# Kernel optimization log

Hardware: AMD Instinct MI355X
Metric: run time of the kernel (lower is better)

The kernel has to match this reference:

```python
import jax, jax.numpy as jnp
import numpy as np

B, T, D, H, F = 4, 2048, 512, 8, 2048
WINDOW = 128
HD = D // H
EPS = 1e-5


def layer_norm(x, g, b):
    mu = jnp.mean(x, axis=-1, keepdims=True)
    var = jnp.mean(jnp.square(x - mu), axis=-1, keepdims=True)
    return (x - mu) * jax.lax.rsqrt(var + EPS) * g + b


def setup_inputs() -> dict:
    key = jax.random.key(0)
    ks = jax.random.split(key, 5)
    s = 0.02
    return {
        "x": jax.random.normal(ks[0], (B, T, D), dtype=jnp.float32),
        "in_proj_w": jax.random.normal(ks[1], (3 * D, D), dtype=jnp.float32) * s,
        "in_proj_b": jnp.zeros((3 * D,), dtype=jnp.float32),
        "out_w": jax.random.normal(ks[2], (D, D), dtype=jnp.float32) * s,
        "out_b": jnp.zeros((D,), dtype=jnp.float32),
        "ln1_g": jnp.ones((D,), dtype=jnp.float32),
        "ln1_b": jnp.zeros((D,), dtype=jnp.float32),
        "ln2_g": jnp.ones((D,), dtype=jnp.float32),
        "ln2_b": jnp.zeros((D,), dtype=jnp.float32),
        "w1": jax.random.normal(ks[3], (F, D), dtype=jnp.float32) * s,
        "b1": jnp.zeros((F,), dtype=jnp.float32),
        "w2": jax.random.normal(ks[4], (D, F), dtype=jnp.float32) * s,
        "b2": jnp.zeros((D,), dtype=jnp.float32),
    }


def reference(x, in_proj_w, in_proj_b, out_w, out_b, ln1_g, ln1_b, ln2_g, ln2_b, w1, b1, w2, b2):
    # pre-norm sliding-window causal self-attention
    x2 = layer_norm(x, ln1_g, ln1_b)
    qkv = x2 @ in_proj_w.T + in_proj_b  # (B,T,3D)
    q, k, v = jnp.split(qkv, 3, axis=-1)
    q = q.reshape(B, T, H, HD)
    k = k.reshape(B, T, H, HD)
    v = v.reshape(B, T, H, HD)
    scale = 1.0 / np.sqrt(HD).astype(np.float32)
    scores = jnp.einsum("bthd,bshd->bhts", q, k) * scale  # dense (B,H,T,T)
    idx = jnp.arange(T)
    i = idx[:, None]
    j = idx[None, :]
    allowed = (j <= i) & (j >= i - WINDOW + 1)  # (T,T) bool, True = attend
    scores = jnp.where(allowed[None, None], scores, -jnp.inf)
    attn = jax.nn.softmax(scores, axis=-1)
    ctx = jnp.einsum("bhts,bshd->bthd", attn, v).reshape(B, T, D)
    attn_out = ctx @ out_w.T + out_b
    x = x + attn_out  # dropout is identity in eval
    # FFN block
    x3 = layer_norm(x, ln2_g, ln2_b)
    h = jax.nn.gelu(x3 @ w1.T + b1, approximate=False)
    x = x + h @ w2.T + b2
    return x
```

## Files before the change

### kernel.cpp

```cpp
#include <hip/hip_runtime.h>
#include <math.h>

constexpr int Bn = 4;
constexpr int Tn = 2048;
constexpr int Dn = 512;
constexpr int Hn = 8;
constexpr int HDn = 64;
constexpr int Fn = 2048;
constexpr int WIN = 128;
constexpr float EPS = 1e-5f;
constexpr int Mrows = Bn * Tn;
constexpr int QKVD = 3 * Dn;

using short8 = __attribute__((ext_vector_type(8))) short;
using f32x4  = __attribute__((ext_vector_type(4))) float;

__device__ __forceinline__ short f2bf(float f) {
    unsigned u = __float_as_uint(f);
    unsigned r = (u + 0x7FFFu + ((u >> 16) & 1u)) >> 16;
    return (short)r;
}

__device__ __forceinline__ float gelu_fast(float v) {
    float u = 1.5957691216f * v * (1.0f + 0.044715f * v * v);
    float t = 1.0f - 2.0f / (__expf(u) + 1.0f);
    return 0.5f * v * (1.0f + t);
}

__device__ __forceinline__ void async16(const short* g, short* l) {
    __builtin_amdgcn_global_load_lds(
        (const __attribute__((address_space(1))) void*)g,
        (__attribute__((address_space(3))) void*)l,
        16, 0, 0);
}

__device__ __forceinline__ void ln_row(const float* __restrict__ xrow,
                                       const float* __restrict__ g,
                                       const float* __restrict__ b,
                                       short* __restrict__ yrow, int lane)
{
    const float4* xr = (const float4*)xrow;
    float4 v0 = xr[lane];
    float4 v1 = xr[lane + 64];
    float s = v0.x + v0.y + v0.z + v0.w + v1.x + v1.y + v1.z + v1.w;
#pragma unroll
    for (int off = 32; off >= 1; off >>= 1) s += __shfl_xor(s, off, 64);
    float mu = s * (1.0f / Dn);
    float d0x = v0.x - mu, d0y = v0.y - mu, d0z = v0.z - mu, d0w = v0.w - mu;
    float d1x = v1.x - mu, d1y = v1.y - mu, d1z = v1.z - mu, d1w = v1.w - mu;
    float q = d0x*d0x + d0y*d0y + d0z*d0z + d0w*d0w
            + d1x*d1x + d1y*d1y + d1z*d1z + d1w*d1w;
#pragma unroll
    for (int off = 32; off >= 1; off >>= 1) q += __shfl_xor(q, off, 64);
    float inv = rsqrtf(q * (1.0f / Dn) + EPS);
    const float4* gr = (const float4*)g;
    const float4* br = (const float4*)b;
    float4 g0 = gr[lane], g1 = gr[lane + 64];
    float4 b0 = br[lane], b1 = br[lane + 64];
    short4 a0, a1;
    a0.x = f2bf(d0x * inv * g0.x + b0.x);
    a0.y = f2bf(d0y * inv * g0.y + b0.y);
    a0.z = f2bf(d0z * inv * g0.z + b0.z);
    a0.w = f2bf(d0w * inv * g0.w + b0.w);
    a1.x = f2bf(d1x * inv * g1.x + b1.x);
    a1.y = f2bf(d1y * inv * g1.y + b1.y);
    a1.z = f2bf(d1z * inv * g1.z + b1.z);
    a1.w = f2bf(d1w * inv * g1.w + b1.w);
    short4* yr = (short4*)yrow;
    yr[lane] = a0;
    yr[lane + 64] = a1;
}

__global__ __launch_bounds__(256) void prep_kernel(const float* __restrict__ s0,
                                                   const float* __restrict__ s1,
                                                   const float* __restrict__ s2,
                                                   const float* __restrict__ s3,
                                                   short* __restrict__ d0,
                                                   short* __restrict__ d1,
                                                   short* __restrict__ d2,
                                                   short* __restrict__ d3,
                                                   const float* __restrict__ x,
                                                   const float* __restrict__ ln1_g,
                                                   const float* __restrict__ ln1_b,
                                                   short* __restrict__ x2)
{
    int bid = blockIdx.x;
    if (bid < 3072) {
        int i = bid * 256 + threadIdx.x;
        const float* src; short* dst; int j;
        if (i < 196608)      { src = s0; dst = d0; j = i; }
        else if (i < 262144) { src = s1; dst = d1; j = i - 196608; }
        else if (i < 524288) { src = s2; dst = d2; j = i - 262144; }
        else                 { src = s3; dst = d3; j = i - 524288; }
        float4 v = ((const float4*)src)[j];
        short4 o;
        o.x = f2bf(v.x); o.y = f2bf(v.y); o.z = f2bf(v.z); o.w = f2bf(v.w);
        ((short4*)dst)[j] = o;
    } else {
        int row = (bid - 3072) * 4 + (threadIdx.x >> 6);
        int lane = threadIdx.x & 63;
        ln_row(x + (size_t)row * Dn, ln1_g, ln1_b, x2 + (size_t)row * Dn, lane);
    }
}

__global__ __launch_bounds__(256) void ln_kernel(const float* __restrict__ x,
                                                 const float* __restrict__ g,
                                                 const float* __restrict__ b,
                                                 short* __restrict__ y)
{
    int row = blockIdx.x * 4 + (threadIdx.x >> 6);
    int lane = threadIdx.x & 63;
    ln_row(x + (size_t)row * Dn, g, b, y + (size_t)row * Dn, lane);
}

__global__ __launch_bounds__(256) void gemm_res(const short* __restrict__ A,
                                                const short* __restrict__ Bw,
                                                const float* __restrict__ bias,
                                                const float* __restrict__ resid,
                                                float* __restrict__ Cf,
                                                int M, int N, int K)
{
    constexpr int BK = 64;
    constexpr int ABUF = 64 * BK;
    constexpr int BBUF = 128 * BK;
    __shared__ short SMEM[2 * (ABUF + BBUF)];
    short* Asb = SMEM;
    short* Bsb = SMEM + 2 * ABUF;

    int tid = threadIdx.x;
    int w = tid >> 6, lane = tid & 63;
    int wr = w >> 1, wc = w & 1;
    int nN = N >> 7;
    int bid = blockIdx.x;
    int xcd = bid & 7, sq = bid >> 3;
    int mi = xcd + 8 * (sq / nN);
    int ni = sq % nN;
    int m0 = mi * 64, n0 = ni * 128;
    int quad = lane >> 4, l16 = lane & 15;

    f32x4 zero = {0.f, 0.f, 0.f, 0.f};
    f32x4 acc[2][4];
#pragma unroll
    for (int i = 0; i < 2; ++i)
#pragma unroll
        for (int j = 0; j < 4; ++j) acc[i][j] = zero;

    int rl = lane >> 3;
    int ch = lane & 7;
    const short* Ag[2];
    const short* Bg[4];
    int aOff[2], bOff[4];
#pragma unroll
    for (int s = 0; s < 2; ++s) {
        int rowl = w * 16 + s * 8 + rl;
        int csw = (ch ^ (rowl & 7)) * 8;
        Ag[s] = A + (size_t)(m0 + rowl) * K + csw;
        aOff[s] = (w * 16 + s * 8) * BK;
    }
#pragma unroll
    for (int s = 0; s < 4; ++s) {
        int rowl = w * 32 + s * 8 + rl;
        int csw = (ch ^ (rowl & 7)) * 8;
        Bg[s] = Bw + (size_t)(n0 + rowl) * K + csw;
        bOff[s] = (w * 32 + s * 8) * BK;
    }

    auto stage = [&](int kt, int pp) {
#pragma unroll
        for (int s = 0; s < 2; ++s)
            async16(Ag[s] + kt, Asb + pp * ABUF + aOff[s]);
#pragma unroll
        for (int s = 0; s < 4; ++s)
            async16(Bg[s] + kt, Bsb + pp * BBUF + bOff[s]);
    };

    int aoff[2], boff[4];
#pragma unroll
    for (int i = 0; i < 2; ++i) {
        int ra = wr * 32 + i * 16 + l16;
        aoff[i] = ra * BK;
    }
#pragma unroll
    for (int j = 0; j < 4; ++j) {
        int rb = wc * 64 + j * 16 + l16;
        boff[j] = rb * BK;
    }

    stage(0, 0);
    int p = 0;
    for (int kt = 0; kt < K; kt += BK) {
        __syncthreads();
        if (kt + BK < K) stage(kt + BK, p ^ 1);
        short8 aF[2][2], bF[2][4];
#pragma unroll
        for (int kk = 0; kk < 2; ++kk) {
#pragma unroll
            for (int i = 0; i < 2; ++i) {
                int ra = wr * 32 + i * 16 + l16;
                int cs = ((kk * 4 + quad) ^ (ra & 7)) * 8;
                aF[kk][i] = *(const short8*)(Asb + p * ABUF + aoff[i] + cs);
            }
#pragma unroll
            for (int j = 0; j < 4; ++j) {
                int rb = wc * 64 + j * 16 + l16;
                int cs = ((kk * 4 + quad) ^ (rb & 7)) * 8;
                bF[kk][j] = *(const short8*)(Bsb + p * BBUF + boff[j] + cs);
            }
        }
#pragma unroll
        for (int kk = 0; kk < 2; ++kk)
#pragma unroll
            for (int i = 0; i < 2; ++i)
#pragma unroll
                for (int j = 0; j < 4; ++j)
                    acc[i][j] = __builtin_amdgcn_mfma_f32_16x16x32_bf16(
                        aF[kk][i], bF[kk][j], acc[i][j], 0, 0, 0);
        p ^= 1;
    }

#pragma unroll
    for (int j = 0; j < 4; ++j) {
        int n = n0 + wc * 64 + j * 16 + l16;
        float bv = bias[n];
#pragma unroll
        for (int i = 0; i < 2; ++i) {
            int mbase = m0 + wr * 32 + i * 16 + quad * 4;
#pragma unroll
            for (int r = 0; r < 4; ++r) {
                size_t idx = (size_t)(mbase + r) * N + n;
                Cf[idx] = acc[i][j][r] + bv + resid[idx];
            }
        }
    }
}

template <int MODE>
__global__ __launch_bounds__(256, 2) void gemm_wide(const short* __restrict__ A,
                                                    const short* __restrict__ Bw,
                                                    const float* __restrict__ bias,
                                                    void* __restrict__ Cout,
                                                    short* __restrict__ q_out,
                                                    short* __restrict__ k_out,
                                                    short* __restrict__ v_out,
                                                    int M, int N, int K)
{
    constexpr int BK = 32;
    constexpr int ABUF = 128 * BK;
    constexpr int BBUF = 256 * BK;
    __shared__ short SMEM[2 * (ABUF + BBUF)];
    short* Asb = SMEM;
    short* Bsb = SMEM + 2 * ABUF;

    int tid = threadIdx.x;
    int w = tid >> 6, lane = tid & 63;
    int wr = w >> 1, wc = w & 1;
    int nT = N >> 8;
    int bid = blockIdx.x;
    int xcd = bid & 7, sq = bid >> 3;
    int mi = xcd + 8 * (sq / nT);
    int ni = sq % nT;
    int m0 = mi * 128, n0 = ni * 256;
    int quad = lane >> 4, l16 = lane & 15;

    f32x4 zero = {0.f, 0.f, 0.f, 0.f};
    f32x4 acc[4][8];
#pragma unroll
    for (int i = 0; i < 4; ++i)
#pragma unroll
        for (int j = 0; j < 8; ++j) acc[i][j] = zero;

    int rl = lane >> 2;
    int ch = lane & 3;
    const short* Ag[2];
    const short* Bg[4];
    int aOff[2], bOff[4];
#pragma unroll
    for (int s = 0; s < 2; ++s) {
        int rowl = w * 32 + s * 16 + rl;
        int csw = (ch ^ ((rowl >> 1) & 3)) * 8;
        Ag[s] = A + (size_t)(m0 + rowl) * K + csw;
        aOff[s] = (w * 32 + s * 16) * BK;
    }
#pragma unroll
    for (int s = 0; s < 4; ++s) {
        int rowl = w * 64 + s * 16 + rl;
        int csw = (ch ^ ((rowl >> 1) & 3)) * 8;
        Bg[s] = Bw + (size_t)(n0 + rowl) * K + csw;
        bOff[s] = (w * 64 + s * 16) * BK;
    }

    auto stage = [&](int kt, int pp) {
#pragma unroll
        for (int s = 0; s < 2; ++s)
            async16(Ag[s] + kt, Asb + pp * ABUF + aOff[s]);
#pragma unroll
        for (int s = 0; s < 4; ++s)
            async16(Bg[s] + kt, Bsb + pp * BBUF + bOff[s]);
    };

    int aoff[4], boff[8];
#pragma unroll
    for (int i = 0; i < 4; ++i) {
        int ra = wr * 64 + i * 16 + l16;
        aoff[i] = ra * BK + (quad ^ ((ra >> 1) & 3)) * 8;
    }
#pragma unroll
    for (int j = 0; j < 8; ++j) {
        int rb = wc * 128 + j * 16 + l16;
        boff[j] = rb * BK + (quad ^ ((rb >> 1) & 3)) * 8;
    }

    stage(0, 0);
    int p = 0;
    for (int kt = 0; kt < K; kt += BK) {
        __syncthreads();
        if (kt + BK < K) stage(kt + BK, p ^ 1);
        short8 aF[4], bF[8];
#pragma unroll
        for (int i = 0; i < 4; ++i)
            aF[i] = *(const short8*)(Asb + p * ABUF + aoff[i]);
#pragma unroll
        for (int j = 0; j < 8; ++j)
            bF[j] = *(const short8*)(Bsb + p * BBUF + boff[j]);
#pragma unroll
        for (int i = 0; i < 4; ++i)
#pragma unroll
            for (int j = 0; j < 8; ++j)
                acc[i][j] = __builtin_amdgcn_mfma_f32_16x16x32_bf16(
                    aF[i], bF[j], acc[i][j], 0, 0, 0);
        p ^= 1;
    }

    __syncthreads();
    short* rp = SMEM + w * 6144;
    float bv[8];
#pragma unroll
    for (int j = 0; j < 8; ++j) bv[j] = bias[n0 + wc * 128 + j * 16 + l16];

    if constexpr (MODE == 2) {
        short* Cb = (short*)Cout;
#pragma unroll
        for (int ph = 0; ph < 2; ++ph) {
#pragma unroll
            for (int i = 2 * ph; i < 2 * ph + 2; ++i) {
                int ml = (i - 2 * ph) * 16 + quad * 4;
#pragma unroll
                for (int j = 0; j < 8; ++j)
#pragma unroll
                    for (int r = 0; r < 4; ++r)
                        rp[(ml + r) * 136 + j * 16 + l16] =
                            f2bf(gelu_fast(acc[i][j][r] + bv[j]));
            }
#pragma unroll
            for (int it = 0; it < 8; ++it) {
                int row = it * 4 + (lane >> 4);
                int off = (lane & 15) * 8;
                *(short8*)(Cb + (size_t)(m0 + wr * 64 + 32 * ph + row) * N
                              + n0 + wc * 128 + off) =
                    *(const short8*)(rp + row * 136 + off);
            }
        }
        return;
    }

    if constexpr (MODE == 3) {
        int b = m0 >> 11;
        int ncol0 = n0 + wc * 128;
        int sec = ncol0 >> 9;
        int h0 = (ncol0 & 511) >> 6;
        int t0 = (m0 & 2047) + wr * 64;
        if (sec == 2) {
#pragma unroll
            for (int ph = 0; ph < 2; ++ph) {
#pragma unroll
                for (int j = 4 * ph; j < 4 * ph + 4; ++j) {
                    int d = (j - 4 * ph) * 16 + l16;
#pragma unroll
                    for (int i = 0; i < 4; ++i)
#pragma unroll
                        for (int r = 0; r < 4; ++r)
                            rp[d * 68 + i * 16 + quad * 4 + r] =
                                f2bf(acc[i][j][r] + bv[j]);
                }
                int bh = b * 8 + h0 + ph;
#pragma unroll
                for (int it = 0; it < 8; ++it) {
                    int drow = it * 8 + (lane >> 3);
                    int off = (lane & 7) * 8;
                    *(short8*)(v_out + ((size_t)bh * 64 + drow) * 2048 + t0 + off) =
                        *(const short8*)(rp + drow * 68 + off);
                }
            }
        } else {
            short* dst = (sec == 0 ? q_out : k_out);
#pragma unroll
            for (int ph = 0; ph < 2; ++ph) {
#pragma unroll
                for (int i = 2 * ph; i < 2 * ph + 2; ++i) {
                    int tl = (i - 2 * ph) * 16 + quad * 4;
#pragma unroll
                    for (int j = 0; j < 8; ++j)
#pragma unroll
                        for (int r = 0; r < 4; ++r)
                            rp[(tl + r) * 136 + j * 16 + l16] =
                                f2bf(acc[i][j][r] + bv[j]);
                }
#pragma unroll
                for (int it = 0; it < 8; ++it) {
                    int trow = it * 4 + (lane >> 4);
                    int hh = (lane & 15) >> 3;
                    int off = (lane & 7) * 8;
                    int bh = b * 8 + h0 + hh;
                    *(short8*)(dst + ((size_t)bh * 2048 + t0 + 32 * ph + trow) * 64 + off) =
                        *(const short8*)(rp + trow * 136 + hh * 64 + off);
                }
            }
        }
        return;
    }
}

constexpr int QS = 72;
constexpr int VS = 200;

__global__ __launch_bounds__(256) void attn_mfma(const short* __restrict__ Qg,
                                                 const short* __restrict__ Kg,
                                                 const short* __restrict__ Vtg,
                                                 short* __restrict__ ctx)
{
    __shared__ short Qs[64 * QS];
    __shared__ short Ks[192 * QS];
    __shared__ short Vt[64 * VS];
    int tid = threadIdx.x;
    int w = tid >> 6, lane = tid & 63, quad = lane >> 4, l16 = lane & 15;
    int blk = blockIdx.x;
    int q0 = (blk & 31) << 6;
    int bh = blk >> 5;
    int kbase = q0 - 128;

    {
        const short* src = Qg + ((size_t)bh * 2048 + q0) * 64;
        for (int c = tid; c < 512; c += 256) {
            int row = c >> 3, off = (c & 7) * 8;
            *(short8*)(Qs + row * QS + off) = *(const short8*)(src + row * 64 + off);
        }
    }
    {
        const short* base = Kg + (size_t)bh * 2048 * 64;
        for (int c = tid; c < 1536; c += 256) {
            int row = c >> 3, off = (c & 7) * 8;
            int srow = kbase + row; srow = srow < 0 ? 0 : srow;
            *(short8*)(Ks + row * QS + off) = *(const short8*)(base + (size_t)srow * 64 + off);
        }
    }
    {
        const short* base = Vtg + (size_t)bh * 64 * 2048;
        for (int c = tid; c < 1536; c += 256) {
            int row = c / 24, cc = c - row * 24;
            int off = cc * 8;
            int scol = kbase + off; scol = scol < 0 ? 0 : scol;
            *(short8*)(Vt + row * VS + off) = *(const short8*)(base + (size_t)row * 2048 + scol);
        }
    }
    __syncthreads();

    short8 aF0 = *(const short8*)(Qs + (w * 16 + l16) * QS + quad * 8);
    short8 aF1 = *(const short8*)(Qs + (w * 16 + l16) * QS + 32 + quad * 8);
    f32x4 S[12];
    f32x4 zero = {0.f, 0.f, 0.f, 0.f};
#pragma unroll
    for (int t = 0; t < 12; ++t) S[t] = zero;
#pragma unroll
    for (int t = 0; t < 12; ++t) {
        short8 b0 = *(const short8*)(Ks + (t * 16 + l16) * QS + quad * 8);
        short8 b1 = *(const short8*)(Ks + (t * 16 + l16) * QS + 32 + quad * 8);
        S[t] = __builtin_amdgcn_mfma_f32_16x16x32_bf16(aF0, b0, S[t], 0, 0, 0);
        S[t] = __builtin_amdgcn_mfma_f32_16x16x32_bf16(aF1, b1, S[t], 0, 0, 0);
    }

    int i0 = w * 16 + quad * 4;
    float mrow[4] = {-INFINITY, -INFINITY, -INFINITY, -INFINITY};
#pragma unroll
    for (int t = 0; t < 12; ++t) {
        int jl = t * 16 + l16;
        int kg = kbase + jl;
#pragma unroll
        for (int r = 0; r < 4; ++r) {
            int dj = jl - (i0 + r);
            bool ok = (dj >= 1) && (dj <= 128) && (kg >= 0);
            float s = ok ? S[t][r] * 0.125f : -INFINITY;
            S[t][r] = s;
            mrow[r] = fmaxf(mrow[r], s);
        }
    }
#pragma unroll
    for (int off = 8; off >= 1; off >>= 1)
#pragma unroll
        for (int r = 0; r < 4; ++r)
            mrow[r] = fmaxf(mrow[r], __shfl_xor(mrow[r], off, 64));
    float sum[4] = {0.f, 0.f, 0.f, 0.f};
#pragma unroll
    for (int t = 0; t < 12; ++t)
#pragma unroll
        for (int r = 0; r < 4; ++r) {
            float p = __expf(S[t][r] - mrow[r]);
            S[t][r] = p;
            sum[r] += p;
        }
#pragma unroll
    for (int off = 8; off >= 1; off >>= 1)
#pragma unroll
        for (int r = 0; r < 4; ++r)
            sum[r] += __shfl_xor(sum[r], off, 64);
    float inv[4];
#pragma unroll
    for (int r = 0; r < 4; ++r) inv[r] = 1.0f / sum[r];

    __syncthreads();
    short* Ps = Ks;
#pragma unroll
    for (int t = 0; t < 12; ++t)
#pragma unroll
        for (int r = 0; r < 4; ++r)
            Ps[(w * 16 + quad * 4 + r) * VS + t * 16 + l16] = f2bf(S[t][r]);

    f32x4 O[4];
#pragma unroll
    for (int tN = 0; tN < 4; ++tN) O[tN] = zero;
#pragma unroll
    for (int s = 0; s < 6; ++s) {
        short8 aP = *(const short8*)(Ps + (w * 16 + l16) * VS + s * 32 + quad * 8);
#pragma unroll
        for (int tN = 0; tN < 4; ++tN) {
            short8 bV = *(const short8*)(Vt + (tN * 16 + l16) * VS + s * 32 + quad * 8);
            O[tN] = __builtin_amdgcn_mfma_f32_16x16x32_bf16(aP, bV, O[tN], 0, 0, 0);
        }
    }

    int b = bh >> 3, h = bh & 7;
#pragma unroll
    for (int tN = 0; tN < 4; ++tN)
#pragma unroll
        for (int r = 0; r < 4; ++r) {
            int trow = q0 + w * 16 + quad * 4 + r;
            ctx[((size_t)(b * 2048 + trow)) * 512 + h * 64 + tN * 16 + l16] =
                f2bf(O[tN][r] * inv[r]);
        }
}

extern "C" void kernel_launch(void* const* d_in, const int* in_sizes, int n_in,
                              void* d_out, int out_size, void* d_ws, size_t ws_size,
                              hipStream_t stream)
{
    const float* x         = (const float*)d_in[0];
    const float* in_proj_w = (const float*)d_in[1];
    const float* in_proj_b = (const float*)d_in[2];
    const float* out_w     = (const float*)d_in[3];
    const float* out_b     = (const float*)d_in[4];
    const float* ln1_g     = (const float*)d_in[5];
    const float* ln1_b     = (const float*)d_in[6];
    const float* ln2_g     = (const float*)d_in[7];
    const float* ln2_b     = (const float*)d_in[8];
    const float* w1        = (const float*)d_in[9];
    const float* b1        = (const float*)d_in[10];
    const float* w2        = (const float*)d_in[11];
    const float* b2        = (const float*)d_in[12];
    float* out = (float*)d_out;

    char* ws = (char*)d_ws;
    short* attnQ = (short*)ws;
    short* attnK = (short*)(ws + (size_t)8 * 1024 * 1024);
    short* attnV = (short*)(ws + (size_t)16 * 1024 * 1024);
    short* hbuf  = (short*)ws;
    short* regB  = (short*)(ws + (size_t)32 * 1024 * 1024);
    short* wq  = (short*)(ws + (size_t)40 * 1024 * 1024);
    short* wo  = wq + (size_t)QKVD * Dn;
    short* w1b = wo + (size_t)Dn * Dn;
    short* w2b = w1b + (size_t)Fn * Dn;

    prep_kernel<<<5120, 256, 0, stream>>>(in_proj_w, out_w, w1, w2, wq, wo, w1b, w2b,
                                          x, ln1_g, ln1_b, regB);
    gemm_wide<3><<<(Mrows / 128) * (QKVD / 256), 256, 0, stream>>>(
        regB, wq, in_proj_b, nullptr, attnQ, attnK, attnV, Mrows, QKVD, Dn);
    attn_mfma<<<Bn * Hn * (Tn / 64), 256, 0, stream>>>(attnQ, attnK, attnV, regB);
    gemm_res<<<(Mrows / 64) * (Dn / 128), 256, 0, stream>>>(
        regB, wo, out_b, x, out, Mrows, Dn, Dn);
    ln_kernel<<<Mrows / 4, 256, 0, stream>>>(out, ln2_g, ln2_b, regB);
    gemm_wide<2><<<(Mrows / 128) * (Fn / 256), 256, 0, stream>>>(
        regB, w1b, b1, hbuf, nullptr, nullptr, nullptr, Mrows, Fn, Dn);
    gemm_res<<<(Mrows / 64) * (Dn / 128), 256, 0, stream>>>(
        hbuf, w2b, b2, out, out, Mrows, Dn, Fn);
}
```

Before: 216.2 us.

## Store post-attention residual in bf16 and split QKV GEMM into smaller tiles

```diff
diff --git a/kernel.cpp b/kernel.cpp
--- a/kernel.cpp
+++ b/kernel.cpp
@@ -19,6 +19,9 @@
     unsigned u = __float_as_uint(f);
     unsigned r = (u + 0x7FFFu + ((u >> 16) & 1u)) >> 16;
     return (short)r;
+}
+__device__ __forceinline__ float bf2f(short s) {
+    return __uint_as_float(((unsigned)(unsigned short)s) << 16);
 }
 
 __device__ __forceinline__ float gelu_fast(float v) {
@@ -103,21 +106,48 @@
     }
 }
 
-__global__ __launch_bounds__(256) void ln_kernel(const float* __restrict__ x,
-                                                 const float* __restrict__ g,
-                                                 const float* __restrict__ b,
-                                                 short* __restrict__ y)
+__global__ __launch_bounds__(256) void ln2_kernel(const short* __restrict__ xh,
+                                                  const float* __restrict__ g,
+                                                  const float* __restrict__ b,
+                                                  short* __restrict__ y)
 {
     int row = blockIdx.x * 4 + (threadIdx.x >> 6);
     int lane = threadIdx.x & 63;
-    ln_row(x + (size_t)row * Dn, g, b, y + (size_t)row * Dn, lane);
-}
-
+    const short* xrow = xh + (size_t)row * Dn;
+    short8 v = *(const short8*)(xrow + lane * 8);
+    float f[8];
+#pragma unroll
+    for (int k = 0; k < 8; ++k) f[k] = bf2f(v[k]);
+    float s = 0.f;
+#pragma unroll
+    for (int k = 0; k < 8; ++k) s += f[k];
+#pragma unroll
+    for (int off = 32; off >= 1; off >>= 1) s += __shfl_xor(s, off, 64);
+    float mu = s * (1.0f / Dn);
+    float q = 0.f;
+#pragma unroll
+    for (int k = 0; k < 8; ++k) { float d = f[k] - mu; q += d * d; }
+#pragma unroll
+    for (int off = 32; off >= 1; off >>= 1) q += __shfl_xor(q, off, 64);
+    float inv = rsqrtf(q * (1.0f / Dn) + EPS);
+    const float4* gr = (const float4*)g;
+    const float4* br = (const float4*)b;
+    float4 g0 = gr[2 * lane], g1 = gr[2 * lane + 1];
+    float4 b0 = br[2 * lane], b1 = br[2 * lane + 1];
+    float gg[8] = {g0.x, g0.y, g0.z, g0.w, g1.x, g1.y, g1.z, g1.w};
+    float bb[8] = {b0.x, b0.y, b0.z, b0.w, b1.x, b1.y, b1.z, b1.w};
+    short8 o;
+#pragma unroll
+    for (int k = 0; k < 8; ++k) o[k] = f2bf((f[k] - mu) * inv * gg[k] + bb[k]);
+    *(short8*)(y + (size_t)row * Dn + lane * 8) = o;
+}
+
+template <int RIN, int OUT>
 __global__ __launch_bounds__(256) void gemm_res(const short* __restrict__ A,
                                                 const short* __restrict__ Bw,
                                                 const float* __restrict__ bias,
-                                                const float* __restrict__ resid,
-                                                float* __restrict__ Cf,
+                                                const void* __restrict__ resid,
+                                                void* __restrict__ Cout,
                                                 int M, int N, int K)
 {
     constexpr int BK = 64;
@@ -174,18 +204,6 @@
             async16(Bg[s] + kt, Bsb + pp * BBUF + bOff[s]);
     };
 
-    int aoff[2], boff[4];
-#pragma unroll
-    for (int i = 0; i < 2; ++i) {
-        int ra = wr * 32 + i * 16 + l16;
-        aoff[i] = ra * BK;
-    }
-#pragma unroll
-    for (int j = 0; j < 4; ++j) {
-        int rb = wc * 64 + j * 16 + l16;
-        boff[j] = rb * BK;
-    }
-
     stage(0, 0);
     int p = 0;
     for (int kt = 0; kt < K; kt += BK) {
@@ -198,13 +216,13 @@
             for (int i = 0; i < 2; ++i) {
                 int ra = wr * 32 + i * 16 + l16;
                 int cs = ((kk * 4 + quad) ^ (ra & 7)) * 8;
-                aF[kk][i] = *(const short8*)(Asb + p * ABUF + aoff[i] + cs);
+                aF[kk][i] = *(const short8*)(Asb + p * ABUF + ra * BK + cs);
             }
 #pragma unroll
             for (int j = 0; j < 4; ++j) {
                 int rb = wc * 64 + j * 16 + l16;
                 int cs = ((kk * 4 + quad) ^ (rb & 7)) * 8;
-                bF[kk][j] = *(const short8*)(Bsb + p * BBUF + boff[j] + cs);
+                bF[kk][j] = *(const short8*)(Bsb + p * BBUF + rb * BK + cs);
             }
         }
 #pragma unroll
@@ -218,30 +236,207 @@
         p ^= 1;
     }
 
-#pragma unroll
-    for (int j = 0; j < 4; ++j) {
-        int n = n0 + wc * 64 + j * 16 + l16;
-        float bv = bias[n];
+    const float* rf = (const float*)resid;
+    const short* rh = (const short*)resid;
+
+    if constexpr (OUT == 0) {
+        float* Cf = (float*)Cout;
+#pragma unroll
+        for (int j = 0; j < 4; ++j) {
+            int n = n0 + wc * 64 + j * 16 + l16;
+            float bv = bias[n];
+#pragma unroll
+            for (int i = 0; i < 2; ++i) {
+                int mbase = m0 + wr * 32 + i * 16 + quad * 4;
+#pragma unroll
+                for (int r = 0; r < 4; ++r) {
+                    size_t idx = (size_t)(mbase + r) * N + n;
+                    float rv = RIN ? bf2f(rh[idx]) : rf[idx];
+                    Cf[idx] = acc[i][j][r] + bv + rv;
+                }
+            }
+        }
+    } else {
+        __syncthreads();
+        short* rp = SMEM + w * 6144;
+#pragma unroll
+        for (int j = 0; j < 4; ++j) {
+            int n = n0 + wc * 64 + j * 16 + l16;
+            float bv = bias[n];
+#pragma unroll
+            for (int i = 0; i < 2; ++i) {
+                int ml = i * 16 + quad * 4;
+#pragma unroll
+                for (int r = 0; r < 4; ++r) {
+                    size_t idx = (size_t)(m0 + wr * 32 + ml + r) * N + n;
+                    float rv = RIN ? bf2f(rh[idx]) : rf[idx];
+                    rp[(ml + r) * 72 + j * 16 + l16] = f2bf(acc[i][j][r] + bv + rv);
+                }
+            }
+        }
+        short* Cb = (short*)Cout;
+#pragma unroll
+        for (int it = 0; it < 4; ++it) {
+            int row = it * 8 + (lane >> 3);
+            int off = (lane & 7) * 8;
+            *(short8*)(Cb + (size_t)(m0 + wr * 32 + row) * N + n0 + wc * 64 + off) =
+                *(const short8*)(rp + row * 72 + off);
+        }
+    }
+}
+
+__global__ __launch_bounds__(256, 3) void gemm_qkv(const short* __restrict__ A,
+                                                   const short* __restrict__ Bw,
+                                                   const float* __restrict__ bias,
+                                                   short* __restrict__ q_out,
+                                                   short* __restrict__ k_out,
+                                                   short* __restrict__ v_out,
+                                                   int M, int N, int K)
+{
+    constexpr int BK = 32;
+    constexpr int ABUF = 64 * BK;
+    constexpr int BBUF = 256 * BK;
+    __shared__ short SMEM[2 * (ABUF + BBUF)];
+    short* Asb = SMEM;
+    short* Bsb = SMEM + 2 * ABUF;
+
+    int tid = threadIdx.x;
+    int w = tid >> 6, lane = tid & 63;
+    int wr = w >> 1, wc = w & 1;
+    int nT = N >> 8;
+    int bid = blockIdx.x;
+    int xcd = bid & 7, sq = bid >> 3;
+    int mi = xcd + 8 * (sq / nT);
+    int ni = sq % nT;
+    int m0 = mi * 64, n0 = ni * 256;
+    int quad = lane >> 4, l16 = lane & 15;
+
+    f32x4 zero = {0.f, 0.f, 0.f, 0.f};
+    f32x4 acc[2][8];
+#pragma unroll
+    for (int i = 0; i < 2; ++i)
+#pragma unroll
+        for (int j = 0; j < 8; ++j) acc[i][j] = zero;
+
+    int rl = lane >> 2;
+    int ch = lane & 3;
+    const short* Ag;
+    const short* Bg[4];
+    int aOff, bOff[4];
+    {
+        int rowl = w * 16 + rl;
+        int csw = (ch ^ ((rowl >> 1) & 3)) * 8;
+        Ag = A + (size_t)(m0 + rowl) * K + csw;
+        aOff = (w * 16) * BK;
+    }
+#pragma unroll
+    for (int s = 0; s < 4; ++s) {
+        int rowl = w * 64 + s * 16 + rl;
+        int csw = (ch ^ ((rowl >> 1) & 3)) * 8;
+        Bg[s] = Bw + (size_t)(n0 + rowl) * K + csw;
+        bOff[s] = (w * 64 + s * 16) * BK;
+    }
+
+    auto stage = [&](int kt, int pp) {
+        async16(Ag + kt, Asb + pp * ABUF + aOff);
+#pragma unroll
+        for (int s = 0; s < 4; ++s)
+            async16(Bg[s] + kt, Bsb + pp * BBUF + bOff[s]);
+    };
+
+    int aoff[2], boff[8];
+#pragma unroll
+    for (int i = 0; i < 2; ++i) {
+        int ra = wr * 32 + i * 16 + l16;
+        aoff[i] = ra * BK + (quad ^ ((ra >> 1) & 3)) * 8;
+    }
+#pragma unroll
+    for (int j = 0; j < 8; ++j) {
+        int rb = wc * 128 + j * 16 + l16;
+        boff[j] = rb * BK + (quad ^ ((rb >> 1) & 3)) * 8;
+    }
+
+    stage(0, 0);
+    int p = 0;
+    for (int kt = 0; kt < K; kt += BK) {
+        __syncthreads();
+        if (kt + BK < K) stage(kt + BK, p ^ 1);
+        short8 aF[2], bF[8];
+#pragma unroll
+        for (int i = 0; i < 2; ++i)
+            aF[i] = *(const short8*)(Asb + p * ABUF + aoff[i]);
+#pragma unroll
+        for (int j = 0; j < 8; ++j)
+            bF[j] = *(const short8*)(Bsb + p * BBUF + boff[j]);
+#pragma unroll
+        for (int i = 0; i < 2; ++i)
+#pragma unroll
+            for (int j = 0; j < 8; ++j)
+                acc[i][j] = __builtin_amdgcn_mfma_f32_16x16x32_bf16(
+                    aF[i], bF[j], acc[i][j], 0, 0, 0);
+        p ^= 1;
+    }
+
+    __syncthreads();
+    short* rp = SMEM + w * 5120;
+    float bv[8];
+#pragma unroll
+    for (int j = 0; j < 8; ++j) bv[j] = bias[n0 + wc * 128 + j * 16 + l16];
+
+    int b = m0 >> 11;
+    int ncol0 = n0 + wc * 128;
+    int sec = ncol0 >> 9;
+    int h0 = (ncol0 & 511) >> 6;
+    int t0 = (m0 & 2047) + wr * 32;
+
+    if (sec == 2) {
+#pragma unroll
+        for (int ph = 0; ph < 2; ++ph) {
+#pragma unroll
+            for (int j = 4 * ph; j < 4 * ph + 4; ++j) {
+                int d = (j - 4 * ph) * 16 + l16;
+#pragma unroll
+                for (int i = 0; i < 2; ++i)
+#pragma unroll
+                    for (int r = 0; r < 4; ++r)
+                        rp[d * 40 + i * 16 + quad * 4 + r] = f2bf(acc[i][j][r] + bv[j]);
+            }
+            int bh = b * 8 + h0 + ph;
+#pragma unroll
+            for (int it = 0; it < 4; ++it) {
+                int drow = it * 16 + (lane >> 2);
+                int toff = (lane & 3) * 8;
+                *(short8*)(v_out + ((size_t)bh * 64 + drow) * 2048 + t0 + toff) =
+                    *(const short8*)(rp + drow * 40 + toff);
+            }
+        }
+    } else {
+        short* dst = (sec == 0 ? q_out : k_out);
 #pragma unroll
         for (int i = 0; i < 2; ++i) {
-            int mbase = m0 + wr * 32 + i * 16 + quad * 4;
-#pragma unroll
-            for (int r = 0; r < 4; ++r) {
-                size_t idx = (size_t)(mbase + r) * N + n;
-                Cf[idx] = acc[i][j][r] + bv + resid[idx];
-            }
-        }
-    }
-}
-
-template <int MODE>
-__global__ __launch_bounds__(256, 2) void gemm_wide(const short* __restrict__ A,
+            int tl = i * 16 + quad * 4;
+#pragma unroll
+            for (int j = 0; j < 8; ++j)
+#pragma unroll
+                for (int r = 0; r < 4; ++r)
+                    rp[(tl + r) * 136 + j * 16 + l16] = f2bf(acc[i][j][r] + bv[j]);
+        }
+#pragma unroll
+        for (int it = 0; it < 8; ++it) {
+            int trow = it * 4 + (lane >> 4);
+            int hh = (lane & 15) >> 3;
+            int off = (lane & 7) * 8;
+            int bh = b * 8 + h0 + hh;
+            *(short8*)(dst + ((size_t)bh * 2048 + t0 + trow) * 64 + off) =
+                *(const short8*)(rp + trow * 136 + hh * 64 + off);
+        }
+    }
+}
+
+__global__ __launch_bounds__(256, 2) void gemm_ffn1(const short* __restrict__ A,
                                                     const short* __restrict__ Bw,
                                                     const float* __restrict__ bias,
-                                                    void* __restrict__ Cout,
-                                                    short* __restrict__ q_out,
-                                                    short* __restrict__ k_out,
-                                                    short* __restrict__ v_out,
+                                                    short* __restrict__ Cb,
                                                     int M, int N, int K)
 {
     constexpr int BK = 32;
@@ -336,87 +531,26 @@
     float bv[8];
 #pragma unroll
     for (int j = 0; j < 8; ++j) bv[j] = bias[n0 + wc * 128 + j * 16 + l16];
-
-    if constexpr (MODE == 2) {
-        short* Cb = (short*)Cout;
-#pragma unroll
-        for (int ph = 0; ph < 2; ++ph) {
-#pragma unroll
-            for (int i = 2 * ph; i < 2 * ph + 2; ++i) {
-                int ml = (i - 2 * ph) * 16 + quad * 4;
-#pragma unroll
-                for (int j = 0; j < 8; ++j)
-#pragma unroll
-                    for (int r = 0; r < 4; ++r)
-                        rp[(ml + r) * 136 + j * 16 + l16] =
-                            f2bf(gelu_fast(acc[i][j][r] + bv[j]));
-            }
-#pragma unroll
-            for (int it = 0; it < 8; ++it) {
-                int row = it * 4 + (lane >> 4);
-                int off = (lane & 15) * 8;
-                *(short8*)(Cb + (size_t)(m0 + wr * 64 + 32 * ph + row) * N
-                              + n0 + wc * 128 + off) =
-                    *(const short8*)(rp + row * 136 + off);
-            }
-        }
-        return;
-    }
-
-    if constexpr (MODE == 3) {
-        int b = m0 >> 11;
-        int ncol0 = n0 + wc * 128;
-        int sec = ncol0 >> 9;
-        int h0 = (ncol0 & 511) >> 6;
-        int t0 = (m0 & 2047) + wr * 64;
-        if (sec == 2) {
-#pragma unroll
-            for (int ph = 0; ph < 2; ++ph) {
-#pragma unroll
-                for (int j = 4 * ph; j < 4 * ph + 4; ++j) {
-                    int d = (j - 4 * ph) * 16 + l16;
-#pragma unroll
-                    for (int i = 0; i < 4; ++i)
-#pragma unroll
-                        for (int r = 0; r < 4; ++r)
-                            rp[d * 68 + i * 16 + quad * 4 + r] =
-                                f2bf(acc[i][j][r] + bv[j]);
-                }
-                int bh = b * 8 + h0 + ph;
-#pragma unroll
-                for (int it = 0; it < 8; ++it) {
-                    int drow = it * 8 + (lane >> 3);
-                    int off = (lane & 7) * 8;
-                    *(short8*)(v_out + ((size_t)bh * 64 + drow) * 2048 + t0 + off) =
-                        *(const short8*)(rp + drow * 68 + off);
-                }
-            }
-        } else {
-            short* dst = (sec == 0 ? q_out : k_out);
-#pragma unroll
-            for (int ph = 0; ph < 2; ++ph) {
-#pragma unroll
-                for (int i = 2 * ph; i < 2 * ph + 2; ++i) {
-                    int tl = (i - 2 * ph) * 16 + quad * 4;
-#pragma unroll
-                    for (int j = 0; j < 8; ++j)
-#pragma unroll
-                        for (int r = 0; r < 4; ++r)
-                            rp[(tl + r) * 136 + j * 16 + l16] =
-                                f2bf(acc[i][j][r] + bv[j]);
-                }
-#pragma unroll
-                for (int it = 0; it < 8; ++it) {
-                    int trow = it * 4 + (lane >> 4);
-                    int hh = (lane & 15) >> 3;
-                    int off = (lane & 7) * 8;
-                    int bh = b * 8 + h0 + hh;
-                    *(short8*)(dst + ((size_t)bh * 2048 + t0 + 32 * ph + trow) * 64 + off) =
-                        *(const short8*)(rp + trow * 136 + hh * 64 + off);
-                }
-            }
-        }
-        return;
+#pragma unroll
+    for (int ph = 0; ph < 2; ++ph) {
+#pragma unroll
+        for (int i = 2 * ph; i < 2 * ph + 2; ++i) {
+            int ml = (i - 2 * ph) * 16 + quad * 4;
+#pragma unroll
+            for (int j = 0; j < 8; ++j)
+#pragma unroll
+                for (int r = 0; r < 4; ++r)
+                    rp[(ml + r) * 136 + j * 16 + l16] =
+                        f2bf(gelu_fast(acc[i][j][r] + bv[j]));
+        }
+#pragma unroll
+        for (int it = 0; it < 8; ++it) {
+            int row = it * 4 + (lane >> 4);
+            int off = (lane & 15) * 8;
+            *(short8*)(Cb + (size_t)(m0 + wr * 64 + 32 * ph + row) * N
+                          + n0 + wc * 128 + off) =
+                *(const short8*)(rp + row * 136 + off);
+        }
     }
 }
 
@@ -577,17 +711,18 @@
     short* wo  = wq + (size_t)QKVD * Dn;
     short* w1b = wo + (size_t)Dn * Dn;
     short* w2b = w1b + (size_t)Fn * Dn;
+    short* res1 = (short*)(ws + (size_t)48 * 1024 * 1024);
 
     prep_kernel<<<5120, 256, 0, stream>>>(in_proj_w, out_w, w1, w2, wq, wo, w1b, w2b,
                                           x, ln1_g, ln1_b, regB);
-    gemm_wide<3><<<(Mrows / 128) * (QKVD / 256), 256, 0, stream>>>(
-        regB, wq, in_proj_b, nullptr, attnQ, attnK, attnV, Mrows, QKVD, Dn);
+    gemm_qkv<<<(Mrows / 64) * (QKVD / 256), 256, 0, stream>>>(
+        regB, wq, in_proj_b, attnQ, attnK, attnV, Mrows, QKVD, Dn);
     attn_mfma<<<Bn * Hn * (Tn / 64), 256, 0, stream>>>(attnQ, attnK, attnV, regB);
-    gemm_res<<<(Mrows / 64) * (Dn / 128), 256, 0, stream>>>(
-        regB, wo, out_b, x, out, Mrows, Dn, Dn);
-    ln_kernel<<<Mrows / 4, 256, 0, stream>>>(out, ln2_g, ln2_b, regB);
-    gemm_wide<2><<<(Mrows / 128) * (Fn / 256), 256, 0, stream>>>(
-        regB, w1b, b1, hbuf, nullptr, nullptr, nullptr, Mrows, Fn, Dn);
-    gemm_res<<<(Mrows / 64) * (Dn / 128), 256, 0, stream>>>(
-        hbuf, w2b, b2, out, out, Mrows, Dn, Fn);
-}
+    gemm_res<0, 1><<<(Mrows / 64) * (Dn / 128), 256, 0, stream>>>(
+        regB, wo, out_b, x, res1, Mrows, Dn, Dn);
+    ln2_kernel<<<Mrows / 4, 256, 0, stream>>>(res1, ln2_g, ln2_b, regB);
+    gemm_ffn1<<<(Mrows / 128) * (Fn / 256), 256, 0, stream>>>(
+        regB, w1b, b1, hbuf, Mrows, Fn, Dn);
+    gemm_res<1, 0><<<(Mrows / 64) * (Dn / 128), 256, 0, stream>>>(
+        hbuf, w2b, b2, res1, out, Mrows, Dn, Fn);
+}
```

Result: no change. 213.5 us (-1.3%).
